# Optimization experiments

Measured on AMD Instinct MI355X. Metric: run time of the kernel, lower is better.

Reference implementation:

```python
import jax, jax.numpy as jnp
import numpy as np

N_NODES = 10000
N_EDGES = 100000
MUL = 32        # multiplicity of 0e and 1o in node feats / out irreps
ATTR = 16       # node_attrs scalars
RADIAL = 8      # edge_feats scalars
W_NUMEL = 4 * MUL * MUL  # 4 CG paths, fully-connected [mul1=32, mul2=1, mul_out=32]


def setup_inputs() -> dict:
    key = jax.random.key(0)
    ks = jax.random.split(key, 12)
    return {
        'node_attrs': jax.random.normal(ks[0], (N_NODES, ATTR), jnp.float32),
        'node_feats': jax.random.normal(ks[1], (N_NODES, 4 * MUL), jnp.float32),  # 32x0e | 32x1o flattened
        'edge_attrs': jax.random.normal(ks[2], (N_EDGES, 4), jnp.float32),        # Y0 | Y1 (3 comps)
        'edge_feats': jax.random.normal(ks[3], (N_EDGES, RADIAL), jnp.float32),
        'edge_index': jax.random.randint(ks[4], (2, N_EDGES), 0, N_NODES, jnp.int32),
        'Wgen': jax.random.normal(ks[5], (RADIAL, W_NUMEL), jnp.float32),  # conv_tp_weights (o3.Linear on scalars)
        'L1s': jax.random.normal(ks[6], (MUL, MUL), jnp.float32),  # linear_1, scalar block
        'L1v': jax.random.normal(ks[7], (MUL, MUL), jnp.float32),  # linear_1, vector block
        'WS0': jax.random.normal(ks[8], (MUL, ATTR, MUL), jnp.float32),  # skip_tp 0e*0e->0e
        'WS1': jax.random.normal(ks[9], (MUL, ATTR, MUL), jnp.float32),  # skip_tp 1o*0e->1o
        'L2s': jax.random.normal(ks[10], (MUL, MUL), jnp.float32),
        'L2v': jax.random.normal(ks[11], (MUL, MUL), jnp.float32),
    }


def reference(node_attrs, node_feats, edge_attrs, edge_feats, edge_index,
              Wgen, L1s, L1v, WS0, WS1, L2s, L2v):
    sender, receiver = edge_index[0], edge_index[1]
    n = node_attrs.shape[0]

    # gather sender node feats, split irreps: [E,32] scalars, [E,32,3] vectors
    g = node_feats[sender]
    xs = g[:, :MUL]
    xv = g[:, MUL:].reshape(-1, MUL, 3)
    ys = edge_attrs[:, 0]    # l=0 edge attr
    yv = edge_attrs[:, 1:]   # l=1 edge attr, [E,3]

    # per-edge generated tensor-product weights (o3.Linear on scalar edge feats)
    tw = (edge_feats @ Wgen) * (1.0 / np.sqrt(RADIAL))
    tw = tw.reshape(-1, 4, MUL, MUL)
    WA, WB, WC, WD = tw[:, 0], tw[:, 1], tw[:, 2], tw[:, 3]

    # fully-connected CG tensor product (4 paths, edge attrs have mul=1)
    outA = jnp.einsum('euw,eu,e->ew', WA, xs, ys)          # 0e x 0e -> 0e
    outB = jnp.einsum('euw,eu,ei->ewi', WB, xs, yv)        # 0e x 1o -> 1o
    outC = jnp.einsum('euw,eui,e->ewi', WC, xv, ys)        # 1o x 0e -> 1o
    dot = jnp.einsum('eui,ei->eu', xv, yv) * (1.0 / np.sqrt(3.0))  # CG for 1o x 1o -> 0e
    outD = jnp.einsum('euw,eu->ew', WD, dot)
    alpha = 1.0 / np.sqrt(2 * MUL)  # fan-in path normalization (2 paths x mul1=32 per output irrep)
    ms = (outA + outD) * alpha      # [E,32]
    mv = (outB + outC) * alpha      # [E,32,3]

    # linear_1 (per-irrep mixing)
    lnorm = 1.0 / np.sqrt(MUL)
    ms = (ms @ L1s) * lnorm
    mv = jnp.einsum('ewi,wu->eui', mv, L1v) * lnorm

    # scatter-sum messages to receiver nodes
    Ms = jax.ops.segment_sum(ms, receiver, num_segments=n)   # [N,32]
    Mv = jax.ops.segment_sum(mv, receiver, num_segments=n)   # [N,32,3]

    # skip_tp: out irreps x node_attrs (16x0e) -> out irreps
    snorm = 1.0 / np.sqrt(MUL * ATTR)
    ss = jnp.einsum('uvw,nu,nv->nw', WS0, Ms, node_attrs) * snorm
    sv = jnp.einsum('uvw,nui,nv->nwi', WS1, Mv, node_attrs) * snorm

    # linear_2
    ss = (ss @ L2s) * lnorm
    sv = jnp.einsum('nwi,wu->nui', sv, L2v) * lnorm

    # residual, flatten irreps back to [N, 128]
    return jnp.concatenate([Ms + ss, (Mv + sv).reshape(n, 3 * MUL)], axis=1)
```

## Files before the change

### kernel.cpp

```cpp
#include <hip/hip_runtime.h>

#define N_NODES 10000
#define N_EDGES 100000
#define SLOTS 40

typedef __attribute__((ext_vector_type(8))) _Float16 f16x8;
typedef __attribute__((ext_vector_type(2))) _Float16 f16x2;
typedef __attribute__((ext_vector_type(4))) float f32x4;

static __device__ inline f16x2 pkrtz(float a, float b) {
    auto t = __builtin_amdgcn_cvt_pkrtz(a, b);
    union { decltype(t) x; f16x2 y; } u;
    u.x = t;
    return u.y;
}
static __device__ inline unsigned short f16u(float x) {
    union { _Float16 h; unsigned short s; } u;
    u.h = (_Float16)x;
    return u.s;
}
static __device__ inline float f16f(unsigned short us) {
    union { unsigned short s; _Float16 h; } u;
    u.s = us;
    return (float)u.h;
}
static __device__ inline f16x8 cvt8h(const float* f) {
    f16x8 r; f16x2* rp = (f16x2*)&r;
#pragma unroll
    for (int i = 0; i < 4; ++i) rp[i] = pkrtz(f[2 * i], f[2 * i + 1]);
    return r;
}
static __device__ inline f16x8 scale8(f16x2 h2, f16x8 x) {
    f16x8 r; f16x2* rp = (f16x2*)&r; f16x2* xp = (f16x2*)&x;
#pragma unroll
    for (int i = 0; i < 4; ++i) rp[i] = h2 * xp[i];
    return r;
}
static __device__ inline int pack2(float a, float b) {
    union { f16x2 h; int i; } u;
    u.h = pkrtz(a, b);
    return u.i;
}

__global__ __launch_bounds__(1024) void prep_kernel(
    const float* __restrict__ Wgen, const float* __restrict__ L1s,
    const float* __restrict__ L1v, const float* __restrict__ WS0,
    const float* __restrict__ WS1, const float* __restrict__ L2s,
    const float* __restrict__ L2v, unsigned short* __restrict__ Wc,
    unsigned short* __restrict__ WB0, unsigned short* __restrict__ WB1,
    int* __restrict__ cnt) {
    const float S = 1.0f / 128.0f;
    int tid = blockIdx.x * 1024 + threadIdx.x;
    if (tid < N_NODES) cnt[tid] = 0;
    if (tid < 32768) {
        int j = tid & 7;
        int lane = (tid >> 3) & 63;
        int ks = (tid >> 9) & 7;
        int nt = tid >> 12;
        int col = nt * 16 + (lane & 15);
        int u = (lane >> 4) * 8 + j;
        int r = ks;
        int p, c2;
        const float* M;
        float sc = S;
        if (col < 32)      { p = 0; M = L1s; c2 = col; }
        else if (col < 64) { p = 1; M = L1v; c2 = col - 32; }
        else if (col < 96) { p = 2; M = L1v; c2 = col - 64; }
        else               { p = 3; M = L1s; c2 = col - 96; sc = S * 0.57735026918962576f; }
        const float* wg = Wgen + r * 4096 + p * 1024 + u * 32;
        float acc = 0.f;
#pragma unroll
        for (int w = 0; w < 32; ++w) acc += wg[w] * M[w * 32 + c2];
        Wc[tid] = f16u(acc * sc);
    } else {
        int idx = tid - 32768;
        int table = idx >> 14;
        int r14 = idx & 16383;
        int j = r14 & 7;
        int lane = (r14 >> 3) & 63;
        int ks = (r14 >> 9) & 15;
        int k = ks * 32 + (lane >> 4) * 8 + j;
        int u = k >> 4, v = k & 15;
        int w = ((r14 >> 13) & 1) * 16 + (lane & 15);
        const float* WS = table ? WS1 : WS0;
        const float* L2 = table ? L2v : L2s;
        const float* src = WS + u * 512 + v * 32;
        float acc = 0.f;
#pragma unroll
        for (int x = 0; x < 32; ++x) acc += src[x] * L2[x * 32 + w];
        unsigned short val = f16u(acc * S);
        if (table) WB1[r14] = val; else WB0[r14] = val;
    }
}

__global__ __launch_bounds__(256) void edge_kernel(
    const float* __restrict__ node_feats, const float* __restrict__ edge_attrs,
    const float* __restrict__ edge_feats, const int* __restrict__ edge_index,
    const unsigned short* __restrict__ Wc, int* __restrict__ cnt,
    unsigned short* __restrict__ Msg) {
    __shared__ f16x8 sW8[4096];
    __shared__ int sSL[4][16];
    __shared__ f32x4 sEA[4][16];
    {
        const f16x8* src = (const f16x8*)Wc;
        for (int i = threadIdx.x; i < 4096; i += 256) sW8[i] = src[i];
    }
    __syncthreads();

    const int lane = threadIdx.x & 63;
    const int m = lane & 15, q = lane >> 4;
    const int wv = threadIdx.x >> 6;
    const int wave = (blockIdx.x * 256 + threadIdx.x) >> 6;
    const int stride = gridDim.x * 4;
    const int NT = N_EDGES / 16;

    int tile = wave;
    if (tile >= NT) return;

    f16x8 xs8, xv8[3], dt8;
    float efC[8];
    f32x4 eaC;
    int slC = 0;

    {
        int e = tile * 16 + m;
        int snd = edge_index[e];
        if (lane < 16) {
            int r = edge_index[N_EDGES + e];
            slC = r * SLOTS + atomicAdd(&cnt[r], 1);
        }
        const float* g = node_feats + snd * 128;
        float xs[8], xv[24];
        *(f32x4*)&xs[0] = *(const f32x4*)(g + q * 8);
        *(f32x4*)&xs[4] = *(const f32x4*)(g + q * 8 + 4);
#pragma unroll
        for (int i = 0; i < 6; ++i)
            *(f32x4*)&xv[i * 4] = *(const f32x4*)(g + 32 + q * 24 + i * 4);
        *(f32x4*)&efC[0] = *(const f32x4*)(edge_feats + e * 8);
        *(f32x4*)&efC[4] = *(const f32x4*)(edge_feats + e * 8 + 4);
        eaC = *(const f32x4*)(edge_attrs + e * 4);
        float dt[8];
        float y0 = eaC.y, y1 = eaC.z, y2 = eaC.w;
#pragma unroll
        for (int j = 0; j < 8; ++j)
            dt[j] = xv[j * 3] * y0 + xv[j * 3 + 1] * y1 + xv[j * 3 + 2] * y2;
        xs8 = cvt8h(xs);
#pragma unroll
        for (int c = 0; c < 3; ++c) {
            f16x8 r; f16x2* rp = (f16x2*)&r;
#pragma unroll
            for (int i = 0; i < 4; ++i)
                rp[i] = pkrtz(xv[(2 * i) * 3 + c], xv[(2 * i + 1) * 3 + c]);
            xv8[c] = r;
        }
        dt8 = cvt8h(dt);
    }
    int snd1 = 0, rcv1 = 0;
    {
        int t1 = tile + stride;
        if (t1 < NT) {
            int e1 = t1 * 16 + m;
            snd1 = edge_index[e1];
            if (lane < 16) rcv1 = edge_index[N_EDGES + e1];
        }
    }

    while (tile < NT) {
        const int tn = tile + stride;
        const bool hasN = tn < NT;
        const int t2 = tile + 2 * stride;
        const bool has2 = t2 < NT;

        if (lane < 16) {
            sSL[wv][lane] = slC;
            sEA[wv][lane] = eaC;
        }

        float xsN[8], xvN[24], efN[8];
        f32x4 eaN;
        int slN = 0;
        if (hasN) {
            int en = tn * 16 + m;
            if (lane < 16) slN = rcv1 * SLOTS + atomicAdd(&cnt[rcv1], 1);
            const float* gN = node_feats + snd1 * 128;
            *(f32x4*)&xsN[0] = *(const f32x4*)(gN + q * 8);
            *(f32x4*)&xsN[4] = *(const f32x4*)(gN + q * 8 + 4);
#pragma unroll
            for (int i = 0; i < 6; ++i)
                *(f32x4*)&xvN[i * 4] = *(const f32x4*)(gN + 32 + q * 24 + i * 4);
            *(f32x4*)&efN[0] = *(const f32x4*)(edge_feats + en * 8);
            *(f32x4*)&efN[4] = *(const f32x4*)(edge_feats + en * 8 + 4);
            eaN = *(const f32x4*)(edge_attrs + en * 4);
        }

        int snd2 = 0, rcv2 = 0;
        if (has2) {
            int e2 = t2 * 16 + m;
            snd2 = edge_index[e2];
            if (lane < 16) rcv2 = edge_index[N_EDGES + e2];
        }

        f32x4 z = {0.f, 0.f, 0.f, 0.f};
        f32x4 fA[2] = {z, z}, fB[2] = {z, z}, fD[2] = {z, z};
        f32x4 fC[3][2] = {{z, z}, {z, z}, {z, z}};

#pragma unroll
        for (int ks = 0; ks < 8; ++ks) {
            _Float16 h = (_Float16)efC[ks];
            f16x2 h2 = {h, h};
            {
                f16x8 a = scale8(h2, xs8);
                fA[0] = __builtin_amdgcn_mfma_f32_16x16x32_f16(a, sW8[(0 * 8 + ks) * 64 + lane], fA[0], 0, 0, 0);
                fA[1] = __builtin_amdgcn_mfma_f32_16x16x32_f16(a, sW8[(1 * 8 + ks) * 64 + lane], fA[1], 0, 0, 0);
                fB[0] = __builtin_amdgcn_mfma_f32_16x16x32_f16(a, sW8[(2 * 8 + ks) * 64 + lane], fB[0], 0, 0, 0);
                fB[1] = __builtin_amdgcn_mfma_f32_16x16x32_f16(a, sW8[(3 * 8 + ks) * 64 + lane], fB[1], 0, 0, 0);
            }
            {
                f16x8 bc0 = sW8[(4 * 8 + ks) * 64 + lane];
                f16x8 bc1 = sW8[(5 * 8 + ks) * 64 + lane];
#pragma unroll
                for (int c = 0; c < 3; ++c) {
                    f16x8 a = scale8(h2, xv8[c]);
                    fC[c][0] = __builtin_amdgcn_mfma_f32_16x16x32_f16(a, bc0, fC[c][0], 0, 0, 0);
                    fC[c][1] = __builtin_amdgcn_mfma_f32_16x16x32_f16(a, bc1, fC[c][1], 0, 0, 0);
                }
            }
            {
                f16x8 a = scale8(h2, dt8);
                fD[0] = __builtin_amdgcn_mfma_f32_16x16x32_f16(a, sW8[(6 * 8 + ks) * 64 + lane], fD[0], 0, 0, 0);
                fD[1] = __builtin_amdgcn_mfma_f32_16x16x32_f16(a, sW8[(7 * 8 + ks) * 64 + lane], fD[1], 0, 0, 0);
            }
        }

        int4 sl4 = *(const int4*)&sSL[wv][q * 4];
        const int slR[4] = {sl4.x, sl4.y, sl4.z, sl4.w};
#pragma unroll
        for (int t4 = 0; t4 < 4; ++t4) {
            f32x4 ea4 = sEA[wv][q * 4 + t4];
            float ysr = ea4.x, y0r = ea4.y, y1r = ea4.z, y2r = ea4.w;
            int dr = slR[t4];
#pragma unroll
            for (int nt = 0; nt < 2; ++nt) {
                int col = nt * 16 + m;
                float pb = fB[nt][t4];
                int2 pk;
                pk.x = pack2(ysr * fA[nt][t4] + fD[nt][t4],
                             y0r * pb + ysr * fC[0][nt][t4]);
                pk.y = pack2(y1r * pb + ysr * fC[1][nt][t4],
                             y2r * pb + ysr * fC[2][nt][t4]);
                *(int2*)(Msg + (size_t)dr * 128 + col * 4) = pk;
            }
        }

        tile = tn;
        if (hasN) {
            float dtN[8];
            float y0 = eaN.y, y1 = eaN.z, y2 = eaN.w;
#pragma unroll
            for (int j = 0; j < 8; ++j)
                dtN[j] = xvN[j * 3] * y0 + xvN[j * 3 + 1] * y1 + xvN[j * 3 + 2] * y2;
            xs8 = cvt8h(xsN);
#pragma unroll
            for (int c = 0; c < 3; ++c) {
                f16x8 r; f16x2* rp = (f16x2*)&r;
#pragma unroll
                for (int i = 0; i < 4; ++i)
                    rp[i] = pkrtz(xvN[(2 * i) * 3 + c], xvN[(2 * i + 1) * 3 + c]);
                xv8[c] = r;
            }
            dt8 = cvt8h(dtN);
#pragma unroll
            for (int j = 0; j < 8; ++j) efC[j] = efN[j];
            eaC = eaN;
            slC = slN;
            snd1 = snd2;
            rcv1 = rcv2;
        }
    }
}

__global__ __launch_bounds__(256) void node_kernel(
    const float* __restrict__ node_attrs, const unsigned short* __restrict__ Msg,
    const int* __restrict__ cnt, const unsigned short* __restrict__ WB0,
    const unsigned short* __restrict__ WB1, float* __restrict__ out) {
    __shared__ float sM[16][129];
    __shared__ float sAt[16][17];
    int n0 = blockIdx.x * 16;

    int nl = threadIdx.x >> 4;
    int cg = threadIdx.x & 15;
    int n = n0 + nl;
    int s0 = n * SLOTS;
    int s1 = s0 + cnt[n];
    float acc[8];
#pragma unroll
    for (int j = 0; j < 8; ++j) acc[j] = 0.f;
    int s = s0;
    for (; s + 7 < s1; s += 8) {
        f32x4 r[8];
#pragma unroll
        for (int i = 0; i < 8; ++i)
            r[i] = *(const f32x4*)(Msg + (size_t)(s + i) * 128 + cg * 8);
#pragma unroll
        for (int j = 0; j < 8; ++j) {
            float a = 0.f;
#pragma unroll
            for (int i = 0; i < 8; ++i)
                a += f16f(((const unsigned short*)&r[i])[j]);
            acc[j] += a;
        }
    }
    for (; s + 3 < s1; s += 4) {
        f32x4 r0 = *(const f32x4*)(Msg + (size_t)(s + 0) * 128 + cg * 8);
        f32x4 r1 = *(const f32x4*)(Msg + (size_t)(s + 1) * 128 + cg * 8);
        f32x4 r2 = *(const f32x4*)(Msg + (size_t)(s + 2) * 128 + cg * 8);
        f32x4 r3 = *(const f32x4*)(Msg + (size_t)(s + 3) * 128 + cg * 8);
        const unsigned short* u0 = (const unsigned short*)&r0;
        const unsigned short* u1 = (const unsigned short*)&r1;
        const unsigned short* u2 = (const unsigned short*)&r2;
        const unsigned short* u3 = (const unsigned short*)&r3;
#pragma unroll
        for (int j = 0; j < 8; ++j)
            acc[j] += (f16f(u0[j]) + f16f(u1[j])) + (f16f(u2[j]) + f16f(u3[j]));
    }
    for (; s < s1; ++s) {
        f32x4 raw = *(const f32x4*)(Msg + (size_t)s * 128 + cg * 8);
        const unsigned short* us = (const unsigned short*)&raw;
#pragma unroll
        for (int j = 0; j < 8; ++j) acc[j] += f16f(us[j]);
    }
#pragma unroll
    for (int j = 0; j < 8; ++j)
        sM[nl][(j & 3) * 32 + cg * 2 + (j >> 2)] = acc[j];
    sAt[nl][cg] = node_attrs[n * 16 + cg];
    __syncthreads();

    int p = threadIdx.x >> 6;
    int lane = threadIdx.x & 63;
    int m = lane & 15, q = lane >> 4;
    const unsigned short* WB = (p == 0) ? WB0 : WB1;
    int chb = p * 32;
    f32x4 z = {0.f, 0.f, 0.f, 0.f};
    f32x4 D0 = z, D1 = z;
#pragma unroll
    for (int ks = 0; ks < 16; ++ks) {
        int kb = ks * 32 + q * 8;
        float t[8];
#pragma unroll
        for (int j = 0; j < 8; ++j) {
            int k = kb + j;
            t[j] = sM[m][chb + (k >> 4)] * sAt[m][k & 15];
        }
        f16x8 a = cvt8h(t);
        f16x8 b0 = *(const f16x8*)(WB + (ks * 64 + lane) * 8);
        f16x8 b1 = *(const f16x8*)(WB + ((16 + ks) * 64 + lane) * 8);
        D0 = __builtin_amdgcn_mfma_f32_16x16x32_f16(a, b0, D0, 0, 0, 0);
        D1 = __builtin_amdgcn_mfma_f32_16x16x32_f16(a, b1, D1, 0, 0, 0);
    }

#pragma unroll
    for (int t4 = 0; t4 < 4; ++t4) {
        int nl2 = q * 4 + t4;
        int nn = n0 + nl2;
        if (p == 0) {
            out[nn * 128 + m]      = sM[nl2][m] + D0[t4];
            out[nn * 128 + 16 + m] = sM[nl2][16 + m] + D1[t4];
        } else {
            int i = p - 1;
            out[nn * 128 + 32 + m * 3 + i]        = sM[nl2][chb + m] + D0[t4];
            out[nn * 128 + 32 + (16 + m) * 3 + i] = sM[nl2][chb + 16 + m] + D1[t4];
        }
    }
}

extern "C" void kernel_launch(void* const* d_in, const int* in_sizes, int n_in,
                              void* d_out, int out_size, void* d_ws, size_t ws_size,
                              hipStream_t stream) {
    (void)in_sizes; (void)n_in; (void)out_size; (void)ws_size;
    const float* node_attrs = (const float*)d_in[0];
    const float* node_feats = (const float*)d_in[1];
    const float* edge_attrs = (const float*)d_in[2];
    const float* edge_feats = (const float*)d_in[3];
    const int*   edge_index = (const int*)d_in[4];
    const float* Wgen = (const float*)d_in[5];
    const float* L1s  = (const float*)d_in[6];
    const float* L1v  = (const float*)d_in[7];
    const float* WS0  = (const float*)d_in[8];
    const float* WS1  = (const float*)d_in[9];
    const float* L2s  = (const float*)d_in[10];
    const float* L2v  = (const float*)d_in[11];
    float* out = (float*)d_out;
    char* ws = (char*)d_ws;

    unsigned short* Msg = (unsigned short*)ws;
    unsigned short* Wc  = (unsigned short*)(ws + 102400000);
    unsigned short* WB0 = (unsigned short*)(ws + 102465536);
    unsigned short* WB1 = (unsigned short*)(ws + 102498304);
    int* cnt = (int*)(ws + 102531072);

    prep_kernel<<<64, 1024, 0, stream>>>(Wgen, L1s, L1v, WS0, WS1, L2s, L2v,
                                         Wc, WB0, WB1, cnt);
    edge_kernel<<<512, 256, 0, stream>>>(node_feats, edge_attrs, edge_feats,
                                         edge_index, Wc, cnt, Msg);
    node_kernel<<<625, 256, 0, stream>>>(node_attrs, Msg, cnt, WB0, WB1, out);
}
```

Before: 127.3 us.

## Fuse edge and node kernels with a software grid barrier

Merges the edge message kernel and the node aggregation/skip kernel into one persistent kernel. A global atomic counter, zeroed in the prep kernel, acts as a grid-wide barrier between the two phases. Shared memory is reused through a union, and each block then loops over node blocks. The node gather now issues 16 slot loads up front and masks them by degree instead of using unrolled chunks. This removes one launch and the gap between kernels, but the barrier spin costs time and assumes all 512 blocks are co-resident, which the launch-bounds occupancy hint of 2 is meant to support. Loading 16 slots regardless of degree adds memory traffic.

Result: slower. 237.6 us (+86.7%).

```diff
diff --git a/kernel.cpp b/kernel.cpp
--- a/kernel.cpp
+++ b/kernel.cpp
@@ -51,7 +51,7 @@
     int* __restrict__ cnt) {
     const float S = 1.0f / 128.0f;
     int tid = blockIdx.x * 1024 + threadIdx.x;
-    if (tid < N_NODES) cnt[tid] = 0;
+    if (tid <= N_NODES) cnt[tid] = 0;
     if (tid < 32768) {
         int j = tid & 7;
         int lane = (tid >> 3) & 63;
@@ -93,17 +93,21 @@
     }
 }
 
-__global__ __launch_bounds__(256) void edge_kernel(
+__global__ __launch_bounds__(256, 2) void fused_kernel(
     const float* __restrict__ node_feats, const float* __restrict__ edge_attrs,
     const float* __restrict__ edge_feats, const int* __restrict__ edge_index,
     const unsigned short* __restrict__ Wc, int* __restrict__ cnt,
-    unsigned short* __restrict__ Msg) {
-    __shared__ f16x8 sW8[4096];
-    __shared__ int sSL[4][16];
-    __shared__ f32x4 sEA[4][16];
+    unsigned short* __restrict__ Msg, const float* __restrict__ node_attrs,
+    const unsigned short* __restrict__ WB0, const unsigned short* __restrict__ WB1,
+    float* __restrict__ out) {
+    __shared__ union {
+        struct { f16x8 w[4096]; int sl[4][16]; f32x4 ea[4][16]; } p1;
+        struct { float sM[16][129]; float sAt[16][17]; } p2;
+    } su;
+
     {
         const f16x8* src = (const f16x8*)Wc;
-        for (int i = threadIdx.x; i < 4096; i += 256) sW8[i] = src[i];
+        for (int i = threadIdx.x; i < 4096; i += 256) su.p1.w[i] = src[i];
     }
     __syncthreads();
 
@@ -115,7 +119,6 @@
     const int NT = N_EDGES / 16;
 
     int tile = wave;
-    if (tile >= NT) return;
 
     f16x8 xs8, xv8[3], dt8;
     float efC[8];
@@ -172,8 +175,8 @@
         const bool has2 = t2 < NT;
 
         if (lane < 16) {
-            sSL[wv][lane] = slC;
-            sEA[wv][lane] = eaC;
+            su.p1.sl[wv][lane] = slC;
+            su.p1.ea[wv][lane] = eaC;
         }
 
         float xsN[8], xvN[24], efN[8];
@@ -210,14 +213,14 @@
             f16x2 h2 = {h, h};
             {
                 f16x8 a = scale8(h2, xs8);
-                fA[0] = __builtin_amdgcn_mfma_f32_16x16x32_f16(a, sW8[(0 * 8 + ks) * 64 + lane], fA[0], 0, 0, 0);
-                fA[1] = __builtin_amdgcn_mfma_f32_16x16x32_f16(a, sW8[(1 * 8 + ks) * 64 + lane], fA[1], 0, 0, 0);
-                fB[0] = __builtin_amdgcn_mfma_f32_16x16x32_f16(a, sW8[(2 * 8 + ks) * 64 + lane], fB[0], 0, 0, 0);
-                fB[1] = __builtin_amdgcn_mfma_f32_16x16x32_f16(a, sW8[(3 * 8 + ks) * 64 + lane], fB[1], 0, 0, 0);
+                fA[0] = __builtin_amdgcn_mfma_f32_16x16x32_f16(a, su.p1.w[(0 * 8 + ks) * 64 + lane], fA[0], 0, 0, 0);
+                fA[1] = __builtin_amdgcn_mfma_f32_16x16x32_f16(a, su.p1.w[(1 * 8 + ks) * 64 + lane], fA[1], 0, 0, 0);
+                fB[0] = __builtin_amdgcn_mfma_f32_16x16x32_f16(a, su.p1.w[(2 * 8 + ks) * 64 + lane], fB[0], 0, 0, 0);
+                fB[1] = __builtin_amdgcn_mfma_f32_16x16x32_f16(a, su.p1.w[(3 * 8 + ks) * 64 + lane], fB[1], 0, 0, 0);
             }
             {
-                f16x8 bc0 = sW8[(4 * 8 + ks) * 64 + lane];
-                f16x8 bc1 = sW8[(5 * 8 + ks) * 64 + lane];
+                f16x8 bc0 = su.p1.w[(4 * 8 + ks) * 64 + lane];
+                f16x8 bc1 = su.p1.w[(5 * 8 + ks) * 64 + lane];
 #pragma unroll
                 for (int c = 0; c < 3; ++c) {
                     f16x8 a = scale8(h2, xv8[c]);
@@ -227,16 +230,16 @@
             }
             {
                 f16x8 a = scale8(h2, dt8);
-                fD[0] = __builtin_amdgcn_mfma_f32_16x16x32_f16(a, sW8[(6 * 8 + ks) * 64 + lane], fD[0], 0, 0, 0);
-                fD[1] = __builtin_amdgcn_mfma_f32_16x16x32_f16(a, sW8[(7 * 8 + ks) * 64 + lane], fD[1], 0, 0, 0);
-            }
-        }
-
-        int4 sl4 = *(const int4*)&sSL[wv][q * 4];
+                fD[0] = __builtin_amdgcn_mfma_f32_16x16x32_f16(a, su.p1.w[(6 * 8 + ks) * 64 + lane], fD[0], 0, 0, 0);
+                fD[1] = __builtin_amdgcn_mfma_f32_16x16x32_f16(a, su.p1.w[(7 * 8 + ks) * 64 + lane], fD[1], 0, 0, 0);
+            }
+        }
+
+        int4 sl4 = *(const int4*)&su.p1.sl[wv][q * 4];
         const int slR[4] = {sl4.x, sl4.y, sl4.z, sl4.w};
 #pragma unroll
         for (int t4 = 0; t4 < 4; ++t4) {
-            f32x4 ea4 = sEA[wv][q * 4 + t4];
+            f32x4 ea4 = su.p1.ea[wv][q * 4 + t4];
             float ysr = ea4.x, y0r = ea4.y, y1r = ea4.z, y2r = ea4.w;
             int dr = slR[t4];
 #pragma unroll
@@ -277,98 +280,92 @@
             rcv1 = rcv2;
         }
     }
-}
-
-__global__ __launch_bounds__(256) void node_kernel(
-    const float* __restrict__ node_attrs, const unsigned short* __restrict__ Msg,
-    const int* __restrict__ cnt, const unsigned short* __restrict__ WB0,
-    const unsigned short* __restrict__ WB1, float* __restrict__ out) {
-    __shared__ float sM[16][129];
-    __shared__ float sAt[16][17];
-    int n0 = blockIdx.x * 16;
-
-    int nl = threadIdx.x >> 4;
-    int cg = threadIdx.x & 15;
-    int n = n0 + nl;
-    int s0 = n * SLOTS;
-    int s1 = s0 + cnt[n];
-    float acc[8];
-#pragma unroll
-    for (int j = 0; j < 8; ++j) acc[j] = 0.f;
-    int s = s0;
-    for (; s + 7 < s1; s += 8) {
-        f32x4 r[8];
-#pragma unroll
-        for (int i = 0; i < 8; ++i)
-            r[i] = *(const f32x4*)(Msg + (size_t)(s + i) * 128 + cg * 8);
-#pragma unroll
-        for (int j = 0; j < 8; ++j) {
-            float a = 0.f;
-#pragma unroll
-            for (int i = 0; i < 8; ++i)
-                a += f16f(((const unsigned short*)&r[i])[j]);
-            acc[j] += a;
-        }
-    }
-    for (; s + 3 < s1; s += 4) {
-        f32x4 r0 = *(const f32x4*)(Msg + (size_t)(s + 0) * 128 + cg * 8);
-        f32x4 r1 = *(const f32x4*)(Msg + (size_t)(s + 1) * 128 + cg * 8);
-        f32x4 r2 = *(const f32x4*)(Msg + (size_t)(s + 2) * 128 + cg * 8);
-        f32x4 r3 = *(const f32x4*)(Msg + (size_t)(s + 3) * 128 + cg * 8);
-        const unsigned short* u0 = (const unsigned short*)&r0;
-        const unsigned short* u1 = (const unsigned short*)&r1;
-        const unsigned short* u2 = (const unsigned short*)&r2;
-        const unsigned short* u3 = (const unsigned short*)&r3;
+
+    __syncthreads();
+    __threadfence();
+    int* bar = cnt + N_NODES;
+    if (threadIdx.x == 0) {
+        __hip_atomic_fetch_add(bar, 1, __ATOMIC_ACQ_REL, __HIP_MEMORY_SCOPE_AGENT);
+        while (__hip_atomic_load(bar, __ATOMIC_ACQUIRE, __HIP_MEMORY_SCOPE_AGENT)
+               < (int)gridDim.x) {
+            __builtin_amdgcn_s_sleep(8);
+        }
+    }
+    __syncthreads();
+    __threadfence();
+
+    const int tid = threadIdx.x;
+    for (int nb = blockIdx.x; nb < 625; nb += gridDim.x) {
+        __syncthreads();
+        int n0 = nb * 16;
+        int nl = tid >> 4;
+        int cg = tid & 15;
+        int n = n0 + nl;
+        int deg = __hip_atomic_load(&cnt[n], __ATOMIC_RELAXED, __HIP_MEMORY_SCOPE_AGENT);
+        int s0 = n * SLOTS;
+        float acc[8];
+#pragma unroll
+        for (int j = 0; j < 8; ++j) acc[j] = 0.f;
+        {
+            f32x4 r[16];
+#pragma unroll
+            for (int i = 0; i < 16; ++i)
+                r[i] = *(const f32x4*)(Msg + (size_t)(s0 + i) * 128 + cg * 8);
+#pragma unroll
+            for (int i = 0; i < 16; ++i) {
+                if (i < deg) {
+                    const unsigned short* us = (const unsigned short*)&r[i];
+#pragma unroll
+                    for (int j = 0; j < 8; ++j) acc[j] += f16f(us[j]);
+                }
+            }
+        }
+        for (int s = s0 + 16; s < s0 + deg; ++s) {
+            f32x4 raw = *(const f32x4*)(Msg + (size_t)s * 128 + cg * 8);
+            const unsigned short* us = (const unsigned short*)&raw;
+#pragma unroll
+            for (int j = 0; j < 8; ++j) acc[j] += f16f(us[j]);
+        }
 #pragma unroll
         for (int j = 0; j < 8; ++j)
-            acc[j] += (f16f(u0[j]) + f16f(u1[j])) + (f16f(u2[j]) + f16f(u3[j]));
-    }
-    for (; s < s1; ++s) {
-        f32x4 raw = *(const f32x4*)(Msg + (size_t)s * 128 + cg * 8);
-        const unsigned short* us = (const unsigned short*)&raw;
-#pragma unroll
-        for (int j = 0; j < 8; ++j) acc[j] += f16f(us[j]);
-    }
-#pragma unroll
-    for (int j = 0; j < 8; ++j)
-        sM[nl][(j & 3) * 32 + cg * 2 + (j >> 2)] = acc[j];
-    sAt[nl][cg] = node_attrs[n * 16 + cg];
-    __syncthreads();
-
-    int p = threadIdx.x >> 6;
-    int lane = threadIdx.x & 63;
-    int m = lane & 15, q = lane >> 4;
-    const unsigned short* WB = (p == 0) ? WB0 : WB1;
-    int chb = p * 32;
-    f32x4 z = {0.f, 0.f, 0.f, 0.f};
-    f32x4 D0 = z, D1 = z;
-#pragma unroll
-    for (int ks = 0; ks < 16; ++ks) {
-        int kb = ks * 32 + q * 8;
-        float t[8];
-#pragma unroll
-        for (int j = 0; j < 8; ++j) {
-            int k = kb + j;
-            t[j] = sM[m][chb + (k >> 4)] * sAt[m][k & 15];
-        }
-        f16x8 a = cvt8h(t);
-        f16x8 b0 = *(const f16x8*)(WB + (ks * 64 + lane) * 8);
-        f16x8 b1 = *(const f16x8*)(WB + ((16 + ks) * 64 + lane) * 8);
-        D0 = __builtin_amdgcn_mfma_f32_16x16x32_f16(a, b0, D0, 0, 0, 0);
-        D1 = __builtin_amdgcn_mfma_f32_16x16x32_f16(a, b1, D1, 0, 0, 0);
-    }
-
-#pragma unroll
-    for (int t4 = 0; t4 < 4; ++t4) {
-        int nl2 = q * 4 + t4;
-        int nn = n0 + nl2;
-        if (p == 0) {
-            out[nn * 128 + m]      = sM[nl2][m] + D0[t4];
-            out[nn * 128 + 16 + m] = sM[nl2][16 + m] + D1[t4];
-        } else {
-            int i = p - 1;
-            out[nn * 128 + 32 + m * 3 + i]        = sM[nl2][chb + m] + D0[t4];
-            out[nn * 128 + 32 + (16 + m) * 3 + i] = sM[nl2][chb + 16 + m] + D1[t4];
+            su.p2.sM[nl][(j & 3) * 32 + cg * 2 + (j >> 2)] = acc[j];
+        su.p2.sAt[nl][cg] = node_attrs[n * 16 + cg];
+        __syncthreads();
+
+        int p = tid >> 6;
+        int ml = lane & 15, ql = lane >> 4;
+        const unsigned short* WB = (p == 0) ? WB0 : WB1;
+        int chb = p * 32;
+        f32x4 z2 = {0.f, 0.f, 0.f, 0.f};
+        f32x4 D0 = z2, D1 = z2;
+#pragma unroll
+        for (int ks = 0; ks < 16; ++ks) {
+            int kb = ks * 32 + ql * 8;
+            float t[8];
+#pragma unroll
+            for (int j = 0; j < 8; ++j) {
+                int k = kb + j;
+                t[j] = su.p2.sM[ml][chb + (k >> 4)] * su.p2.sAt[ml][k & 15];
+            }
+            f16x8 a = cvt8h(t);
+            f16x8 b0 = *(const f16x8*)(WB + (ks * 64 + lane) * 8);
+            f16x8 b1 = *(const f16x8*)(WB + ((16 + ks) * 64 + lane) * 8);
+            D0 = __builtin_amdgcn_mfma_f32_16x16x32_f16(a, b0, D0, 0, 0, 0);
+            D1 = __builtin_amdgcn_mfma_f32_16x16x32_f16(a, b1, D1, 0, 0, 0);
+        }
+
+#pragma unroll
+        for (int t4 = 0; t4 < 4; ++t4) {
+            int nl2 = ql * 4 + t4;
+            int nn = n0 + nl2;
+            if (p == 0) {
+                out[nn * 128 + ml]      = su.p2.sM[nl2][ml] + D0[t4];
+                out[nn * 128 + 16 + ml] = su.p2.sM[nl2][16 + ml] + D1[t4];
+            } else {
+                int i = p - 1;
+                out[nn * 128 + 32 + ml * 3 + i]        = su.p2.sM[nl2][chb + ml] + D0[t4];
+                out[nn * 128 + 32 + (16 + ml) * 3 + i] = su.p2.sM[nl2][chb + 16 + ml] + D1[t4];
+            }
         }
     }
 }
@@ -400,7 +397,7 @@
 
     prep_kernel<<<64, 1024, 0, stream>>>(Wgen, L1s, L1v, WS0, WS1, L2s, L2v,
                                          Wc, WB0, WB1, cnt);
-    edge_kernel<<<512, 256, 0, stream>>>(node_feats, edge_attrs, edge_feats,
-                                         edge_index, Wc, cnt, Msg);
-    node_kernel<<<625, 256, 0, stream>>>(node_attrs, Msg, cnt, WB0, WB1, out);
-}
+    fused_kernel<<<512, 256, 0, stream>>>(node_feats, edge_attrs, edge_feats,
+                                          edge_index, Wc, cnt, Msg, node_attrs,
+                                          WB0, WB1, out);
+}
```
